# Optimization experiments

Hardware: AMD Instinct MI355X
Metric: run time of the kernel (lower is better)

The kernel has to match this reference:

```python
import jax, jax.numpy as jnp
import numpy as np

B, S, H = 8, 2048, 256

def setup_inputs() -> dict:
    key = jax.random.key(0)
    ks = jax.random.split(key, 7)
    sc = 0.05
    return {
        "inputs": jax.random.normal(ks[0], (B, S, H), dtype=jnp.float32),
        "Wq": jax.random.normal(ks[1], (H, H), dtype=jnp.float32) * sc,
        "bq": jax.random.normal(ks[2], (H,), dtype=jnp.float32) * sc,
        "Wk": jax.random.normal(ks[3], (H, H), dtype=jnp.float32) * sc,
        "bk": jax.random.normal(ks[4], (H,), dtype=jnp.float32) * sc,
        "Wv": jax.random.normal(ks[5], (H, H), dtype=jnp.float32) * sc,
        "bv": jax.random.normal(ks[6], (H,), dtype=jnp.float32) * sc,
    }

def reference(inputs, Wq, bq, Wk, bk, Wv, bv):
    # nn.Linear: y = x @ W.T + b
    q = jnp.einsum("bsh,oh->bso", inputs, Wq) + bq
    k = jnp.einsum("bsh,oh->bso", inputs, Wk) + bk
    v = jnp.einsum("bsh,oh->bso", inputs, Wv) + bv
    hidden = q.shape[-1]
    # NOTE: original scales by sqrt(hidden^2) == hidden (not sqrt(hidden))
    scores = jnp.einsum("bqh,bkh->bqk", q, k) / jnp.float32(hidden)
    # NOTE: original applies softmax over dim=1 (the query axis), not the last axis
    weights = jax.nn.softmax(scores, axis=1)
    return jnp.einsum("bqk,bkh->bqh", weights, v)
```

## Files before the change

### kernel.cpp

```cpp
#include <hip/hip_runtime.h>
#include <hip/hip_bf16.h>

#define B_ 8
#define S_ 2048
#define H_ 256
#define BS_ (B_*S_)

typedef __attribute__((ext_vector_type(8))) short bf16x8;
typedef __attribute__((ext_vector_type(4))) short bf16x4;
typedef __attribute__((ext_vector_type(4))) float f32x4;

static __device__ inline short f2bf(float f) {
  union { float f; unsigned int u; } a; a.f = f;
  unsigned int u = a.u;
  unsigned int r = (u + 0x7fffu + ((u >> 16) & 1u)) >> 16;
  return (short)r;
}

static __device__ inline float bf2f(short s) {
  union { float f; unsigned int u; } a;
  a.u = ((unsigned int)(unsigned short)s) << 16;
  return a.f;
}

static __device__ inline f32x4 mfma16(bf16x8 a, bf16x8 b, f32x4 c) {
  return __builtin_amdgcn_mfma_f32_16x16x32_bf16(a, b, c, 0, 0, 0);
}

static __device__ inline void gl_lds16(const short* g, short* l) {
  __builtin_amdgcn_global_load_lds(
      (const __attribute__((address_space(1))) void*)g,
      (__attribute__((address_space(3))) void*)l, 16, 0, 0);
}

#define NX4 (BS_ * H_ / 4)
#define NW4 (H_ * H_ / 4)
#define NTOT4 (NX4 + 3 * NW4)
#define NALL4 (NTOT4 + BS_ / 4)

__global__ __launch_bounds__(256) void cvt_bf16(
    const float* __restrict__ x,
    const float* __restrict__ Wq, const float* __restrict__ Wk,
    const float* __restrict__ Wv,
    short* __restrict__ xb, short* __restrict__ wqb,
    short* __restrict__ wkb, short* __restrict__ wvb,
    float* __restrict__ den)
{
  int stride = gridDim.x * blockDim.x;
  for (int i = blockIdx.x * blockDim.x + threadIdx.x; i < NALL4; i += stride) {
    if (i >= NTOT4) {
      float4 z = {0.f, 0.f, 0.f, 0.f};
      *(float4*)(den + (size_t)(i - NTOT4) * 4) = z;
      continue;
    }
    const float* src; short* dst; int off;
    if (i < NX4) { src = x; dst = xb; off = i; }
    else {
      int j = i - NX4;
      int w = j >> 14;
      off = j & (NW4 - 1);
      src = (w == 0) ? Wq : (w == 1) ? Wk : Wv;
      dst = (w == 0) ? wqb : (w == 1) ? wkb : wvb;
    }
    float4 v = *(const float4*)(src + off * 4);
    bf16x4 p;
    p[0] = f2bf(v.x); p[1] = f2bf(v.y); p[2] = f2bf(v.z); p[3] = f2bf(v.w);
    *(bf16x4*)(dst + off * 4) = p;
  }
}

__global__ __launch_bounds__(256) void qkv_proj(
    const short* __restrict__ x,
    const short* __restrict__ Wq, const float* __restrict__ bq,
    const short* __restrict__ Wk, const float* __restrict__ bk,
    const short* __restrict__ Wv, const float* __restrict__ bv,
    short* __restrict__ Qo, short* __restrict__ Ko, short* __restrict__ VTo)
{
  const int tid  = threadIdx.x;
  const int wave = tid >> 6;
  const int lane = tid & 63;
  const int quad = lane >> 4;
  const int l16  = lane & 15;
  const int y    = blockIdx.y;

  const short* W    = (y == 0) ? Wq : (y == 1) ? Wk : Wv;
  const float* bias = (y == 0) ? bq : (y == 1) ? bk : bv;
  const int sblk = blockIdx.x * 64;

  __shared__ short wbuf[16 * 512];
  __shared__ short xbuf[4 * 512];

  f32x4 zero = {0.f, 0.f, 0.f, 0.f};
  f32x4 acc[4][4];
#pragma unroll
  for (int i = 0; i < 4; i++)
#pragma unroll
    for (int j = 0; j < 4; j++) acc[i][j] = zero;

  for (int ch = 0; ch < 8; ch++) {
#pragma unroll
    for (int i = 0; i < 4; i++) {
      int r = wave * 4 + i;
      gl_lds16(W + (r * 16 + l16) * H_ + ch * 32 + quad * 8, wbuf + r * 512);
    }
    gl_lds16(x + (sblk + wave * 16 + l16) * H_ + ch * 32 + quad * 8,
             xbuf + wave * 512);
    __syncthreads();
    bf16x8 af[4];
#pragma unroll
    for (int st = 0; st < 4; st++)
      af[st] = *(const bf16x8*)(xbuf + st * 512 + lane * 8);
#pragma unroll
    for (int i = 0; i < 4; i++) {
      bf16x8 bb = *(const bf16x8*)(wbuf + (wave * 4 + i) * 512 + lane * 8);
#pragma unroll
      for (int st = 0; st < 4; st++)
        acc[st][i] = mfma16(af[st], bb, acc[st][i]);
    }
    __syncthreads();
  }

  if (y < 2) {
    short* dst = (y == 0) ? Qo : Ko;
#pragma unroll
    for (int i = 0; i < 4; i++) {
      int col = (wave * 4 + i) * 16 + l16;
      float bvl = bias[col];
#pragma unroll
      for (int st = 0; st < 4; st++) {
#pragma unroll
        for (int r = 0; r < 4; r++) {
          int row = sblk + st * 16 + quad * 4 + r;
          dst[row * H_ + col] = f2bf(acc[st][i][r] + bvl);
        }
      }
    }
  } else {
#pragma unroll
    for (int i = 0; i < 4; i++) {
      int col = (wave * 4 + i) * 16 + l16;
      float bvl = bias[col];
#pragma unroll
      for (int st = 0; st < 4; st++) {
        int row0  = sblk + st * 16 + quad * 4;
        int b_idx = row0 >> 11;
        int k0    = row0 & (S_ - 1);
        bf16x4 pk;
#pragma unroll
        for (int r = 0; r < 4; r++) pk[r] = f2bf(acc[st][i][r] + bvl);
        *(bf16x4*)(VTo + (size_t)b_idx * H_ * S_ + (size_t)col * S_ + k0) = pk;
      }
    }
  }
}

__global__ __launch_bounds__(256, 2) void scores(
    const short* __restrict__ Q, const short* __restrict__ K,
    short* __restrict__ Pf, float* __restrict__ den)
{
  const int tid  = threadIdx.x;
  const int wave = tid >> 6;
  const int lane = tid & 63;
  const int quad = lane >> 4;
  const int l16  = lane & 15;
  const int ktg = blockIdx.x & 3;
  const int qt  = (blockIdx.x >> 2) & 15;
  const int b   = blockIdx.x >> 6;

  const short* Qb = Q + b * S_ * H_;
  const short* Kb = K + b * S_ * H_;
  const int qcol0 = qt * 128;

  __shared__ short qbuf[64 * 512];

  bf16x8 kreg[2][2][8];
  {
    const short* kb = Kb + ((ktg * 4) * 128 + wave * 32 + l16) * H_ + quad * 8;
#pragma unroll
    for (int kf = 0; kf < 2; kf++)
#pragma unroll
      for (int ch = 0; ch < 8; ch++)
        kreg[0][kf][ch] = *(const bf16x8*)(kb + kf * 16 * H_ + ch * 32);
  }

#pragma unroll
  for (int i = 0; i < 16; i++) {
    int region = wave * 16 + i;
    int qf = region >> 3;
    int ch = region & 7;
    gl_lds16(Qb + (qcol0 + qf * 16 + l16) * H_ + ch * 32 + quad * 8,
             qbuf + region * 512);
  }
  __syncthreads();

  const int quadA = quad >> 1;
  const int j0    = (quad & 1) * 4;

#pragma unroll
  for (int t = 0; t < 4; t++) {
    if (t < 3) {
      const short* kb = Kb + ((ktg * 4 + t + 1) * 128 + wave * 32 + l16) * H_ + quad * 8;
#pragma unroll
      for (int kf = 0; kf < 2; kf++)
#pragma unroll
        for (int ch = 0; ch < 8; ch++)
          kreg[(t + 1) & 1][kf][ch] = *(const bf16x8*)(kb + kf * 16 * H_ + ch * 32);
    }

    f32x4 zero = {0.f, 0.f, 0.f, 0.f};
    f32x4 acc[2][8];
#pragma unroll
    for (int i = 0; i < 2; i++)
#pragma unroll
      for (int j = 0; j < 8; j++) acc[i][j] = zero;

#pragma unroll
    for (int ch = 0; ch < 8; ch++) {
#pragma unroll
      for (int qf = 0; qf < 8; qf++) {
        bf16x8 bq = *(const bf16x8*)(qbuf + (qf * 8 + ch) * 512 + lane * 8);
        acc[0][qf] = mfma16(kreg[t & 1][0][ch], bq, acc[0][qf]);
        acc[1][qf] = mfma16(kreg[t & 1][1][ch], bq, acc[1][qf]);
      }
    }

    const int kt    = ktg * 4 + t;
    const int krow0 = kt * 128 + wave * 32;
    const int kw    = krow0 >> 5;

    float rs[2][4] = {{0.f,0.f,0.f,0.f},{0.f,0.f,0.f,0.f}};
#pragma unroll
    for (int kf = 0; kf < 2; kf++) {
#pragma unroll
      for (int qf = 0; qf < 8; qf++) {
        bf16x4 pk;
#pragma unroll
        for (int r = 0; r < 4; r++) {
          float e = __expf(acc[kf][qf][r] * (1.0f / H_));
          rs[kf][r] += e;
          pk[r] = f2bf(e);
        }
        size_t tile = ((size_t)(b * 128 + qt * 8 + qf) << 6) + kw;
        *(bf16x4*)(Pf + (tile << 9) + ((2 * kf + quadA) * 16 + l16) * 8 + j0) = pk;
      }
    }

#pragma unroll
    for (int kf = 0; kf < 2; kf++) {
#pragma unroll
      for (int r = 0; r < 4; r++) {
        float v = rs[kf][r];
        v += __shfl_xor(v, 1, 64);
        v += __shfl_xor(v, 2, 64);
        v += __shfl_xor(v, 4, 64);
        v += __shfl_xor(v, 8, 64);
        if (l16 == 0)
          atomicAdd(&den[b * S_ + krow0 + kf * 16 + quad * 4 + r], v);
      }
    }
  }
}

__global__ __launch_bounds__(256) void vscale(
    short* __restrict__ VT, const float* __restrict__ den)
{
  int i = blockIdx.x * 256 + threadIdx.x;
  int b  = i >> 17;
  int k0 = (i & 511) << 2;
  float4 df = *(const float4*)(den + b * S_ + k0);
  bf16x4 v = *(bf16x4*)(VT + (size_t)i * 4);
  bf16x4 o;
  o[0] = f2bf(bf2f(v[0]) / df.x);
  o[1] = f2bf(bf2f(v[1]) / df.y);
  o[2] = f2bf(bf2f(v[2]) / df.z);
  o[3] = f2bf(bf2f(v[3]) / df.w);
  *(bf16x4*)(VT + (size_t)i * 4) = o;
}

__global__ __launch_bounds__(256) void pv(
    const short* __restrict__ Pf, const short* __restrict__ VTs,
    float* __restrict__ out)
{
  const int tid  = threadIdx.x;
  const int wave = tid >> 6;
  const int lane = tid & 63;
  const int quad = lane >> 4;
  const int l16  = lane & 15;
  const int bx = blockIdx.x;
  const int qt = bx >> 4;
  const int b  = (bx >> 1) & 7;
  const int hs = bx & 1;

  __shared__ short vbuf[32 * 512];
  __shared__ short abuf[16 * 512];

  const int qt16 = qt * 4 + wave;
  const short* VTb = VTs + (size_t)b * H_ * S_ + (size_t)(hs * 128) * S_;
  const size_t tilebase = ((size_t)(b * 128 + qt16) * 64) << 9;

  f32x4 zero = {0.f, 0.f, 0.f, 0.f};
  f32x4 acc[8];
#pragma unroll
  for (int i = 0; i < 8; i++) acc[i] = zero;

  for (int kc = 0; kc < S_; kc += 128) {
#pragma unroll
    for (int i = 0; i < 8; i++) {
      int id = wave * 8 + i;
      int n  = id >> 2;
      int kw = id & 3;
      const short* g = VTb + (size_t)(n * 16 + l16) * S_ + kc + kw * 32 + quad * 8;
      gl_lds16(g, vbuf + id * 512);
    }
#pragma unroll
    for (int kwi = 0; kwi < 4; kwi++) {
      const short* g = Pf + tilebase + (size_t)((kc >> 5) + kwi) * 512 + lane * 8;
      gl_lds16(g, abuf + (wave * 4 + kwi) * 512);
    }
    __syncthreads();
#pragma unroll
    for (int kw = 0; kw < 4; kw++) {
      bf16x8 a = *(const bf16x8*)(abuf + (wave * 4 + kw) * 512 + lane * 8);
#pragma unroll
      for (int n = 0; n < 8; n++) {
        bf16x8 vb = *(const bf16x8*)(vbuf + (n * 4 + kw) * 512 + lane * 8);
        acc[n] = mfma16(a, vb, acc[n]);
      }
    }
    __syncthreads();
  }

  const int q0 = qt16 * 16;
#pragma unroll
  for (int n = 0; n < 8; n++) {
    int col = hs * 128 + n * 16 + l16;
#pragma unroll
    for (int r = 0; r < 4; r++) {
      int q = q0 + quad * 4 + r;
      out[((size_t)b * S_ + q) * H_ + col] = acc[n][r];
    }
  }
}

extern "C" void kernel_launch(void* const* d_in, const int* in_sizes, int n_in,
                              void* d_out, int out_size, void* d_ws, size_t ws_size,
                              hipStream_t stream) {
  const float* x  = (const float*)d_in[0];
  const float* Wq = (const float*)d_in[1];
  const float* bq = (const float*)d_in[2];
  const float* Wk = (const float*)d_in[3];
  const float* bk = (const float*)d_in[4];
  const float* Wv = (const float*)d_in[5];
  const float* bv = (const float*)d_in[6];

  short* xb  = (short*)d_ws;
  short* wqb = xb  + (size_t)BS_ * H_;
  short* wkb = wqb + H_ * H_;
  short* wvb = wkb + H_ * H_;
  short* Qs  = wvb + H_ * H_;
  short* Ks  = Qs  + (size_t)BS_ * H_;
  short* VT  = Ks  + (size_t)BS_ * H_;
  short* P   = VT  + (size_t)BS_ * H_;
  float* den = (float*)(P + (size_t)B_ * S_ * S_);
  float* outp = (float*)d_out;

  cvt_bf16<<<1024, 256, 0, stream>>>(x, Wq, Wk, Wv, xb, wqb, wkb, wvb, den);
  qkv_proj<<<dim3(BS_ / 64, 3), 256, 0, stream>>>(xb, wqb, bq, wkb, bk, wvb, bv, Qs, Ks, VT);
  scores<<<512, 256, 0, stream>>>(Qs, Ks, P, den);
  vscale<<<4096, 256, 0, stream>>>(VT, den);
  pv<<<512, 256, 0, stream>>>(P, VT, outp);
}
```

Before: 185.1 us.

## Double-buffer LDS staging in qkv_proj and pv, load P directly to registers

Both qkv_proj and pv now use ping-pong LDS buffers, so the global-to-LDS loads for the next K chunk are issued before the MFMAs on the current chunk. The two loops are fully unrolled. In pv the P tiles are read straight from global memory into registers instead of going through LDS. This hides load latency behind compute, at the cost of more LDS per block (pv goes to 64KB), which may lower occupancy, and more register pressure.

```diff
diff --git a/kernel.cpp b/kernel.cpp
--- a/kernel.cpp
+++ b/kernel.cpp
@@ -87,8 +87,10 @@
   const float* bias = (y == 0) ? bq : (y == 1) ? bk : bv;
   const int sblk = blockIdx.x * 64;
 
-  __shared__ short wbuf[16 * 512];
-  __shared__ short xbuf[4 * 512];
+  __shared__ short wbufA[16 * 512];
+  __shared__ short xbufA[4 * 512];
+  __shared__ short wbufB[16 * 512];
+  __shared__ short xbufB[4 * 512];
 
   f32x4 zero = {0.f, 0.f, 0.f, 0.f};
   f32x4 acc[4][4];
@@ -97,28 +99,44 @@
 #pragma unroll
     for (int j = 0; j < 4; j++) acc[i][j] = zero;
 
-  for (int ch = 0; ch < 8; ch++) {
-#pragma unroll
-    for (int i = 0; i < 4; i++) {
-      int r = wave * 4 + i;
-      gl_lds16(W + (r * 16 + l16) * H_ + ch * 32 + quad * 8, wbuf + r * 512);
-    }
-    gl_lds16(x + (sblk + wave * 16 + l16) * H_ + ch * 32 + quad * 8,
-             xbuf + wave * 512);
+#define QKV_STAGE(wb, xb_, ch)                                            \
+  {                                                                       \
+    _Pragma("unroll")                                                     \
+    for (int i = 0; i < 4; i++) {                                         \
+      int r = wave * 4 + i;                                               \
+      gl_lds16(W + (r * 16 + l16) * H_ + (ch) * 32 + quad * 8, (wb) + r * 512); \
+    }                                                                     \
+    gl_lds16(x + (sblk + wave * 16 + l16) * H_ + (ch) * 32 + quad * 8,    \
+             (xb_) + wave * 512);                                         \
+  }
+
+#define QKV_MFMA(wb, xb_)                                                 \
+  {                                                                       \
+    bf16x8 af[4];                                                         \
+    _Pragma("unroll")                                                     \
+    for (int st = 0; st < 4; st++)                                        \
+      af[st] = *(const bf16x8*)((xb_) + st * 512 + lane * 8);             \
+    _Pragma("unroll")                                                     \
+    for (int i = 0; i < 4; i++) {                                         \
+      bf16x8 bb = *(const bf16x8*)((wb) + (wave * 4 + i) * 512 + lane * 8); \
+      _Pragma("unroll")                                                   \
+      for (int st = 0; st < 4; st++)                                      \
+        acc[st][i] = mfma16(af[st], bb, acc[st][i]);                      \
+    }                                                                     \
+  }
+
+  QKV_STAGE(wbufA, xbufA, 0);
+#pragma unroll
+  for (int i2 = 0; i2 < 4; i2++) {
     __syncthreads();
-    bf16x8 af[4];
-#pragma unroll
-    for (int st = 0; st < 4; st++)
-      af[st] = *(const bf16x8*)(xbuf + st * 512 + lane * 8);
-#pragma unroll
-    for (int i = 0; i < 4; i++) {
-      bf16x8 bb = *(const bf16x8*)(wbuf + (wave * 4 + i) * 512 + lane * 8);
-#pragma unroll
-      for (int st = 0; st < 4; st++)
-        acc[st][i] = mfma16(af[st], bb, acc[st][i]);
-    }
+    QKV_STAGE(wbufB, xbufB, 2 * i2 + 1);
+    QKV_MFMA(wbufA, xbufA);
     __syncthreads();
-  }
+    if (i2 < 3) QKV_STAGE(wbufA, xbufA, 2 * i2 + 2);
+    QKV_MFMA(wbufB, xbufB);
+  }
+#undef QKV_STAGE
+#undef QKV_MFMA
 
   if (y < 2) {
     short* dst = (y == 0) ? Qo : Ko;
@@ -291,8 +309,8 @@
   const int b  = (bx >> 1) & 7;
   const int hs = bx & 1;
 
-  __shared__ short vbuf[32 * 512];
-  __shared__ short abuf[16 * 512];
+  __shared__ short vbufA[32 * 512];
+  __shared__ short vbufB[32 * 512];
 
   const int qt16 = qt * 4 + wave;
   const short* VTb = VTs + (size_t)b * H_ * S_ + (size_t)(hs * 128) * S_;
@@ -303,32 +321,57 @@
 #pragma unroll
   for (int i = 0; i < 8; i++) acc[i] = zero;
 
-  for (int kc = 0; kc < S_; kc += 128) {
-#pragma unroll
-    for (int i = 0; i < 8; i++) {
-      int id = wave * 8 + i;
-      int n  = id >> 2;
-      int kw = id & 3;
-      const short* g = VTb + (size_t)(n * 16 + l16) * S_ + kc + kw * 32 + quad * 8;
-      gl_lds16(g, vbuf + id * 512);
-    }
-#pragma unroll
-    for (int kwi = 0; kwi < 4; kwi++) {
-      const short* g = Pf + tilebase + (size_t)((kc >> 5) + kwi) * 512 + lane * 8;
-      gl_lds16(g, abuf + (wave * 4 + kwi) * 512);
-    }
+  bf16x8 pregA[4], pregB[4];
+
+#define PV_STAGE_V(vb, kc)                                                  \
+  {                                                                         \
+    _Pragma("unroll")                                                       \
+    for (int i = 0; i < 8; i++) {                                           \
+      int id = wave * 8 + i;                                                \
+      int n  = id >> 2;                                                     \
+      int kw = id & 3;                                                      \
+      const short* g = VTb + (size_t)(n * 16 + l16) * S_ + (kc) + kw * 32 + quad * 8; \
+      gl_lds16(g, (vb) + id * 512);                                         \
+    }                                                                       \
+  }
+
+#define PV_LOAD_P(pr, kc)                                                   \
+  {                                                                         \
+    _Pragma("unroll")                                                       \
+    for (int kwi = 0; kwi < 4; kwi++)                                       \
+      pr[kwi] = *(const bf16x8*)(Pf + tilebase + (size_t)(((kc) >> 5) + kwi) * 512 + lane * 8); \
+  }
+
+#define PV_MFMA(vb, pr)                                                     \
+  {                                                                         \
+    _Pragma("unroll")                                                       \
+    for (int kw = 0; kw < 4; kw++) {                                        \
+      _Pragma("unroll")                                                     \
+      for (int n = 0; n < 8; n++) {                                         \
+        bf16x8 vvb = *(const bf16x8*)((vb) + (n * 4 + kw) * 512 + lane * 8); \
+        acc[n] = mfma16(pr[kw], vvb, acc[n]);                               \
+      }                                                                     \
+    }                                                                       \
+  }
+
+  PV_STAGE_V(vbufA, 0);
+  PV_LOAD_P(pregA, 0);
+#pragma unroll
+  for (int i2 = 0; i2 < 8; i2++) {
     __syncthreads();
-#pragma unroll
-    for (int kw = 0; kw < 4; kw++) {
-      bf16x8 a = *(const bf16x8*)(abuf + (wave * 4 + kw) * 512 + lane * 8);
-#pragma unroll
-      for (int n = 0; n < 8; n++) {
-        bf16x8 vb = *(const bf16x8*)(vbuf + (n * 4 + kw) * 512 + lane * 8);
-        acc[n] = mfma16(a, vb, acc[n]);
-      }
-    }
+    PV_STAGE_V(vbufB, (2 * i2 + 1) * 128);
+    PV_LOAD_P(pregB, (2 * i2 + 1) * 128);
+    PV_MFMA(vbufA, pregA);
     __syncthreads();
-  }
+    if (i2 < 7) {
+      PV_STAGE_V(vbufA, (2 * i2 + 2) * 128);
+      PV_LOAD_P(pregA, (2 * i2 + 2) * 128);
+    }
+    PV_MFMA(vbufB, pregB);
+  }
+#undef PV_STAGE_V
+#undef PV_LOAD_P
+#undef PV_MFMA
 
   const int q0 = qt16 * 16;
 #pragma unroll
```

After: 185.6 us. Within noise of the previous version (+0.3%).
